# Performance work log

Hardware: AMD Instinct MI355X
Metric: run time of the kernel (lower is better)

## Reference

```python
import jax, jax.numpy as jnp
import numpy as np

N_HEADS = 8
N_POINTS = 4


def _bilinear_sample(img, x, y):
    """img: (d, H, W); x, y: (P, H, W) float pixel coords (align_corners=True).
    Zero padding for out-of-bounds (matches F.grid_sample defaults).
    Returns (d, P, H, W)."""
    Hh, Ww = img.shape[1], img.shape[2]
    x0f = jnp.floor(x); y0f = jnp.floor(y)
    x0 = x0f.astype(jnp.int32); x1 = x0 + 1
    y0 = y0f.astype(jnp.int32); y1 = y0 + 1
    wx = x - x0f; wy = y - y0f

    def gather(yi, xi):
        valid = (yi >= 0) & (yi < Hh) & (xi >= 0) & (xi < Ww)
        yc = jnp.clip(yi, 0, Hh - 1)
        xc = jnp.clip(xi, 0, Ww - 1)
        v = img[:, yc, xc]  # (d, P, H, W)
        return v * valid[None].astype(img.dtype)

    out = (gather(y0, x0) * ((1 - wy) * (1 - wx))[None]
           + gather(y0, x1) * ((1 - wy) * wx)[None]
           + gather(y1, x0) * (wy * (1 - wx))[None]
           + gather(y1, x1) * (wy * wx)[None])
    return out


def _forward(query, key, W_off, b_off, W_proj, b_proj):
    B, C, H, W = query.shape
    nh, npts = N_HEADS, N_POINTS
    dh = C // nh
    N = H * W

    # offsets + weights from flattened query tokens
    qf = query.reshape(B, C, N).transpose(0, 2, 1)            # (B, N, C)
    ow = qf @ W_off + b_off                                    # (B, N, nh*npts*3)
    ow = ow.reshape(B, H, W, nh, npts, 3)
    offsets = ow[..., :2]                                      # (B,H,W,nh,npts,2)
    weights = jax.nn.softmax(ow[..., 2], axis=-1)              # (B,H,W,nh,npts)

    # base grid in [-1, 1], (x, y) order
    gy = jnp.linspace(-1.0, 1.0, H, dtype=query.dtype)
    gx = jnp.linspace(-1.0, 1.0, W, dtype=query.dtype)
    gyy, gxx = jnp.meshgrid(gy, gx, indexing='ij')             # (H, W)
    grid = jnp.stack([gxx, gyy], axis=-1)                      # (H, W, 2)

    locs = grid[None, :, :, None, None, :] + offsets * 0.1     # (B,H,W,nh,npts,2)
    locs = locs.transpose(0, 3, 4, 1, 2, 5)                    # (B,nh,npts,H,W,2)
    locs = locs.reshape(B * nh, npts, H, W, 2)

    # normalized -> pixel coords (align_corners=True)
    xpix = (locs[..., 0] + 1.0) * 0.5 * (W - 1)                # (B*nh, npts, H, W)
    ypix = (locs[..., 1] + 1.0) * 0.5 * (H - 1)

    key_r = key.reshape(B * nh, dh, H, W)
    sampled = jax.vmap(_bilinear_sample)(key_r, xpix, ypix)    # (B*nh, dh, npts, H, W)
    sampled = sampled.reshape(B, nh, dh, npts, H, W).transpose(0, 1, 3, 2, 4, 5)  # (B,nh,npts,dh,H,W)

    w = weights.transpose(0, 3, 4, 1, 2)[:, :, :, None, :, :]  # (B,nh,npts,1,H,W)
    out_feat = (sampled * w).sum(axis=2)                       # (B,nh,dh,H,W)
    out_feat = out_feat.reshape(B, C, N).transpose(0, 2, 1)    # (B,N,C)
    return out_feat @ W_proj + b_proj                          # (B,N,C)


def setup_inputs() -> dict:
    key0 = jax.random.key(0)
    ks = jax.random.split(key0, 6)
    B, C, H, W = 8, 256, 64, 64
    query = jax.random.normal(ks[0], (B, C, H, W), dtype=jnp.float32)
    key = jax.random.normal(ks[1], (B, C, H, W), dtype=jnp.float32)
    # small random offset net so sampling deviates from base grid (orig inits to 0)
    W_off = jax.random.normal(ks[2], (C, N_HEADS * N_POINTS * 3), dtype=jnp.float32) * 0.01
    b_off = jax.random.normal(ks[3], (N_HEADS * N_POINTS * 3,), dtype=jnp.float32) * 0.01
    W_proj = jax.random.normal(ks[4], (C, C), dtype=jnp.float32) * (1.0 / np.sqrt(C))
    b_proj = jnp.zeros((C,), dtype=jnp.float32)
    return {"query": query, "key": key, "W_off": W_off, "b_off": b_off,
            "W_proj": W_proj, "b_proj": b_proj}


def reference(query, key, W_off, b_off, W_proj, b_proj):
    return _forward(query, key, W_off, b_off, W_proj, b_proj)
```

## Files before the change

kernel.cpp:

```cpp
#include <hip/hip_runtime.h>

#define NH   8
#define NPTS 4
#define BB   8
#define CCH  256
#define HH   64
#define WW   64
#define NPIX 4096
#define DH   32

__global__ __launch_bounds__(256)
void kA_gemm(const float* __restrict__ query, const float* __restrict__ W_off,
             const float* __restrict__ b_off, float4* __restrict__ coords)
{
    __shared__ float a_lds[32][68];
    __shared__ float w_lds[32][100];

    const int t  = threadIdx.x;
    const int m0 = blockIdx.x * 64;
    const int b  = m0 >> 12;
    const int n0 = m0 & (NPIX - 1);
    const float* qbase = query + (size_t)b * CCH * NPIX + n0;

    const int tm = t >> 3;
    const int tj = t & 7;

    float acc[2][12];
#pragma unroll
    for (int i = 0; i < 2; ++i)
#pragma unroll
        for (int j = 0; j < 12; ++j) acc[i][j] = 0.f;

    for (int kc = 0; kc < CCH; kc += 32) {
        float4 a[2];
#pragma unroll
        for (int ii = 0; ii < 2; ++ii) {
            const int idx = t + ii * 256;
            a[ii] = *(const float4*)(qbase + (size_t)(kc + (idx >> 4)) * NPIX
                                     + ((idx & 15) << 2));
        }
        float4 w[3];
#pragma unroll
        for (int ii = 0; ii < 3; ++ii) {
            const int idx = t + ii * 256;
            const int kk = idx / 24, q = idx - kk * 24;
            w[ii] = *(const float4*)(W_off + (size_t)(kc + kk) * 96 + (q << 2));
        }
        __syncthreads();
#pragma unroll
        for (int ii = 0; ii < 2; ++ii) {
            const int idx = t + ii * 256;
            *(float4*)&a_lds[idx >> 4][(idx & 15) << 2] = a[ii];
        }
#pragma unroll
        for (int ii = 0; ii < 3; ++ii) {
            const int idx = t + ii * 256;
            const int kk = idx / 24, q = idx - kk * 24;
            *(float4*)&w_lds[kk][q << 2] = w[ii];
        }
        __syncthreads();
#pragma unroll
        for (int k = 0; k < 32; ++k) {
            const float2 av = *(const float2*)&a_lds[k][tm << 1];
            const float4 w0 = *(const float4*)&w_lds[k][tj * 12];
            const float4 w1 = *(const float4*)&w_lds[k][tj * 12 + 4];
            const float4 w2 = *(const float4*)&w_lds[k][tj * 12 + 8];
            const float ar[2]  = {av.x, av.y};
            const float wr[12] = {w0.x, w0.y, w0.z, w0.w,
                                  w1.x, w1.y, w1.z, w1.w,
                                  w2.x, w2.y, w2.z, w2.w};
#pragma unroll
            for (int i = 0; i < 2; ++i)
#pragma unroll
                for (int j = 0; j < 12; ++j)
                    acc[i][j] = fmaf(ar[i], wr[j], acc[i][j]);
        }
    }

    float bo[12];
#pragma unroll
    for (int j = 0; j < 12; ++j) bo[j] = b_off[tj * 12 + j];

#pragma unroll
    for (int i = 0; i < 2; ++i) {
        const int g = m0 + (tm << 1) + i;
        const int n = g & (NPIX - 1);
        const float fx = (float)(n & 63), fy = (float)(n >> 6);

        float ox[4], oy[4], l[4];
#pragma unroll
        for (int p = 0; p < 4; ++p) {
            ox[p] = acc[i][p * 3 + 0] + bo[p * 3 + 0];
            oy[p] = acc[i][p * 3 + 1] + bo[p * 3 + 1];
            l[p]  = acc[i][p * 3 + 2] + bo[p * 3 + 2];
        }
        float m = fmaxf(fmaxf(l[0], l[1]), fmaxf(l[2], l[3]));
        float e[4], s = 0.f;
#pragma unroll
        for (int p = 0; p < 4; ++p) { e[p] = __expf(l[p] - m); s += e[p]; }
        const float inv = 1.f / s;

        float4* cp = coords + ((size_t)g * NH + tj) * NPTS;
#pragma unroll
        for (int p = 0; p < 4; ++p)
            cp[p] = make_float4(fx + ox[p] * 3.15f, fy + oy[p] * 3.15f,
                                e[p] * inv, 0.f);
    }
}

__global__ __launch_bounds__(256)
void kT_transpose(const float* __restrict__ key, float* __restrict__ keyT)
{
    __shared__ float tile[64][65];
    int bid = blockIdx.x;
    const int nt = bid & 63; bid >>= 6;
    const int ct = bid & 3;  bid >>= 2;
    const int b  = bid;
    const int n0 = nt * 64, c0 = ct * 64;
    const int t = threadIdx.x;

    const float* src = key + ((size_t)b * CCH + c0) * NPIX + n0;
#pragma unroll
    for (int ii = 0; ii < 4; ++ii) {
        int idx = t + ii * 256;
        int cc = idx >> 4, q = idx & 15;
        float4 v = *(const float4*)(src + (size_t)cc * NPIX + (q << 2));
        tile[cc][(q << 2) + 0] = v.x;
        tile[cc][(q << 2) + 1] = v.y;
        tile[cc][(q << 2) + 2] = v.z;
        tile[cc][(q << 2) + 3] = v.w;
    }
    __syncthreads();
    float* dst = keyT + ((size_t)(b * NPIX + n0)) * CCH + c0;
#pragma unroll
    for (int ii = 0; ii < 4; ++ii) {
        int idx = t + ii * 256;
        int nn = idx >> 4, q = idx & 15;
        float4 v = make_float4(tile[(q << 2) + 0][nn], tile[(q << 2) + 1][nn],
                               tile[(q << 2) + 2][nn], tile[(q << 2) + 3][nn]);
        *(float4*)(dst + (size_t)nn * CCH + (q << 2)) = v;
    }
}

__global__ __launch_bounds__(256)
void kB_gather(const float* __restrict__ keyT, const float4* __restrict__ coords,
               float* __restrict__ feat)
{
    const int bid  = blockIdx.x;
    const int sbid = (bid & 7) * 1024 + (bid >> 3);

    const int t  = threadIdx.x;
    const int wv = t >> 6, l = t & 63;
    const int g  = sbid * 4 + wv;
    const int b  = g >> 12;
    const int head = l >> 3;
    const int cl   = (l & 7) << 2;
    const int c    = head * DH + cl;

    const float*  kb = keyT + (((size_t)b << 12)) * CCH;
    const float4* cp = coords + ((size_t)g * NH + head) * NPTS;

    float4 acc = make_float4(0.f, 0.f, 0.f, 0.f);
#pragma unroll
    for (int pt = 0; pt < 4; ++pt) {
        float4 co = cp[pt];
        float xp = co.x, yp = co.y, wgt = co.z;
        float x0f = floorf(xp), y0f = floorf(yp);
        int   x0  = (int)x0f,  y0  = (int)y0f;
        float wx  = xp - x0f,  wy  = yp - y0f;
#pragma unroll
        for (int cr = 0; cr < 4; ++cr) {
            int   xi = x0 + (cr & 1);
            int   yi = y0 + (cr >> 1);
            float wc = ((cr & 1) ? wx : 1.f - wx) * ((cr >> 1) ? wy : 1.f - wy);
            bool  valid = (xi >= 0) && (xi < WW) && (yi >= 0) && (yi < HH);
            int   xc = min(max(xi, 0), WW - 1);
            int   yc = min(max(yi, 0), HH - 1);
            float ww = valid ? (wgt * wc) : 0.f;
            float4 v = *(const float4*)(kb + ((size_t)((yc << 6) + xc)) * CCH + c);
            acc.x = fmaf(ww, v.x, acc.x);
            acc.y = fmaf(ww, v.y, acc.y);
            acc.z = fmaf(ww, v.z, acc.z);
            acc.w = fmaf(ww, v.w, acc.w);
        }
    }
    *(float4*)(feat + (size_t)g * CCH + c) = acc;
}

__global__ __launch_bounds__(256)
void kB_sample(const float* __restrict__ key, const float4* __restrict__ coords,
               float* __restrict__ feat)
{
    __shared__ float cx[4][64], cy[4][64], cw[4][64];

    const int t = threadIdx.x;
    int bi = blockIdx.x;
    const int y    = bi & 63; bi >>= 6;
    const int head = bi & 7;  bi >>= 3;
    const int b    = bi;

    {
        const int xx = t >> 2, pt = t & 3;
        float4 v = coords[((size_t)(b * NPIX + y * WW + xx) * NH + head) * NPTS + pt];
        cx[pt][xx] = v.x; cy[pt][xx] = v.y; cw[pt][xx] = v.z;
    }
    __syncthreads();

    const int x  = t & 63;
    const int cg = t >> 6;
    const int c0 = head * DH + cg * 8;
    const float* kbase = key + ((size_t)b * CCH + c0) * NPIX;

    float acc[8];
#pragma unroll
    for (int i = 0; i < 8; ++i) acc[i] = 0.f;

#pragma unroll
    for (int pt = 0; pt < 4; ++pt) {
        float xp = cx[pt][x], yp = cy[pt][x], wgt = cw[pt][x];
        float x0f = floorf(xp), y0f = floorf(yp);
        int   x0  = (int)x0f,  y0  = (int)y0f;
        float wx  = xp - x0f,  wy  = yp - y0f;
#pragma unroll
        for (int cr = 0; cr < 4; ++cr) {
            int   xi = x0 + (cr & 1);
            int   yi = y0 + (cr >> 1);
            float wc = ((cr & 1) ? wx : 1.f - wx) * ((cr >> 1) ? wy : 1.f - wy);
            bool  valid = (xi >= 0) && (xi < WW) && (yi >= 0) && (yi < HH);
            int   xc = min(max(xi, 0), WW - 1);
            int   yc = min(max(yi, 0), HH - 1);
            const float* p = kbase + yc * WW + xc;
            float ww = valid ? (wgt * wc) : 0.f;
#pragma unroll
            for (int c = 0; c < 8; ++c)
                acc[c] = fmaf(ww, p[(size_t)c * NPIX], acc[c]);
        }
    }

    float* fp = feat + (size_t)(b * NPIX + y * WW + x) * CCH + c0;
    *(float4*)fp       = make_float4(acc[0], acc[1], acc[2], acc[3]);
    *(float4*)(fp + 4) = make_float4(acc[4], acc[5], acc[6], acc[7]);
}

__global__ __launch_bounds__(256)
void kC_proj(const float* __restrict__ feat, const float* __restrict__ W_proj,
             const float* __restrict__ b_proj, float* __restrict__ out)
{
    __shared__ float a_lds[32][68];
    __shared__ float b_lds[32][128];

    const int t  = threadIdx.x;
    const int mb = blockIdx.x >> 1;
    const int nb = blockIdx.x & 1;
    const int m0 = mb * 64, n0 = nb * 128;

    const int tm = t >> 4, tn = t & 15;
    const int ra = t >> 3, qa = t & 7;
    const int kb = t >> 5, qb = t & 31;

    float acc[4][8];
#pragma unroll
    for (int i = 0; i < 4; ++i)
#pragma unroll
        for (int j = 0; j < 8; ++j) acc[i][j] = 0.f;

    for (int kc = 0; kc < 256; kc += 32) {
        float4 a[2];
#pragma unroll
        for (int ii = 0; ii < 2; ++ii)
            a[ii] = *(const float4*)(feat + (size_t)(m0 + ra + ii * 32) * 256 + kc + (qa << 2));
        float4 w[4];
#pragma unroll
        for (int ii = 0; ii < 4; ++ii)
            w[ii] = *(const float4*)(W_proj + (size_t)(kc + kb + ii * 8) * 256 + n0 + (qb << 2));
        __syncthreads();
#pragma unroll
        for (int ii = 0; ii < 2; ++ii) {
            const int r = ra + ii * 32;
            a_lds[(qa << 2) + 0][r] = a[ii].x;
            a_lds[(qa << 2) + 1][r] = a[ii].y;
            a_lds[(qa << 2) + 2][r] = a[ii].z;
            a_lds[(qa << 2) + 3][r] = a[ii].w;
        }
#pragma unroll
        for (int ii = 0; ii < 4; ++ii)
            *(float4*)&b_lds[kb + ii * 8][qb << 2] = w[ii];
        __syncthreads();
#pragma unroll
        for (int k = 0; k < 32; ++k) {
            float4 av  = *(const float4*)&a_lds[k][tm << 2];
            float4 bv0 = *(const float4*)&b_lds[k][tn << 2];
            float4 bv1 = *(const float4*)&b_lds[k][64 + (tn << 2)];
            float ar[4] = {av.x, av.y, av.z, av.w};
            float br[8] = {bv0.x, bv0.y, bv0.z, bv0.w, bv1.x, bv1.y, bv1.z, bv1.w};
#pragma unroll
            for (int i = 0; i < 4; ++i)
#pragma unroll
                for (int j = 0; j < 8; ++j)
                    acc[i][j] = fmaf(ar[i], br[j], acc[i][j]);
        }
    }

    const float4 bp0 = *(const float4*)(b_proj + n0 + (tn << 2));
    const float4 bp1 = *(const float4*)(b_proj + n0 + 64 + (tn << 2));
#pragma unroll
    for (int i = 0; i < 4; ++i) {
        float* op = out + (size_t)(m0 + (tm << 2) + i) * 256 + n0;
        *(float4*)(op + (tn << 2)) =
            make_float4(acc[i][0] + bp0.x, acc[i][1] + bp0.y,
                        acc[i][2] + bp0.z, acc[i][3] + bp0.w);
        *(float4*)(op + 64 + (tn << 2)) =
            make_float4(acc[i][4] + bp1.x, acc[i][5] + bp1.y,
                        acc[i][6] + bp1.z, acc[i][7] + bp1.w);
    }
}

extern "C" void kernel_launch(void* const* d_in, const int* in_sizes, int n_in,
                              void* d_out, int out_size, void* d_ws, size_t ws_size,
                              hipStream_t stream)
{
    const float* query  = (const float*)d_in[0];
    const float* key    = (const float*)d_in[1];
    const float* W_off  = (const float*)d_in[2];
    const float* b_off  = (const float*)d_in[3];
    const float* W_proj = (const float*)d_in[4];
    const float* b_proj = (const float*)d_in[5];
    float* out = (float*)d_out;

    const size_t keyT_bytes   = (size_t)BB * NPIX * CCH * sizeof(float);
    const size_t coords_bytes = (size_t)BB * NPIX * NH * NPTS * sizeof(float4);
    const size_t feat_bytes   = (size_t)BB * NPIX * CCH * sizeof(float);

    if (ws_size >= keyT_bytes + coords_bytes + feat_bytes) {
        float*  keyT   = (float*)d_ws;
        float4* coords = (float4*)((char*)d_ws + keyT_bytes);
        float*  feat   = (float*)((char*)d_ws + keyT_bytes + coords_bytes);

        kA_gemm<<<(BB * NPIX) / 64, 256, 0, stream>>>(query, W_off, b_off, coords);
        kT_transpose<<<BB * 4 * 64, 256, 0, stream>>>(key, keyT);
        kB_gather<<<(BB * NPIX) / 4, 256, 0, stream>>>(keyT, coords, feat);
        kC_proj<<<(BB * NPIX / 64) * 2, 256, 0, stream>>>(feat, W_proj, b_proj, out);
    } else {
        float4* coords = (float4*)d_ws;
        float*  feat   = (float*)((char*)d_ws + coords_bytes);

        kA_gemm<<<(BB * NPIX) / 64, 256, 0, stream>>>(query, W_off, b_off, coords);
        kB_sample<<<BB * NH * HH, 256, 0, stream>>>(key, coords, feat);
        kC_proj<<<(BB * NPIX / 64) * 2, 256, 0, stream>>>(feat, W_proj, b_proj, out);
    }
}
```

Baseline: 257.1 us.

## Split-K offset GEMM across half-blocks and remap block order in both GEMMs

```diff
diff --git a/kernel.cpp b/kernel.cpp
--- a/kernel.cpp
+++ b/kernel.cpp
@@ -13,98 +13,132 @@
 void kA_gemm(const float* __restrict__ query, const float* __restrict__ W_off,
              const float* __restrict__ b_off, float4* __restrict__ coords)
 {
-    __shared__ float a_lds[32][68];
-    __shared__ float w_lds[32][100];
-
-    const int t  = threadIdx.x;
-    const int m0 = blockIdx.x * 64;
-    const int b  = m0 >> 12;
-    const int n0 = m0 & (NPIX - 1);
+    __shared__ float a_lds[64][68];
+    __shared__ float w_lds[64][100];
+
+    const int t    = threadIdx.x;
+    const int bid  = blockIdx.x;
+    const int sbid = (bid & 7) * 64 + (bid >> 3);
+    const int m0   = sbid * 64;
+    const int b    = m0 >> 12;
+    const int n0   = m0 & (NPIX - 1);
     const float* qbase = query + (size_t)b * CCH * NPIX + n0;
 
-    const int tm = t >> 3;
-    const int tj = t & 7;
-
-    float acc[2][12];
-#pragma unroll
-    for (int i = 0; i < 2; ++i)
+    const int kg = t >> 7;
+    const int tl = t & 127;
+    const int tm = tl >> 3;
+    const int tj = tl & 7;
+
+    float acc[4][12];
+#pragma unroll
+    for (int i = 0; i < 4; ++i)
 #pragma unroll
         for (int j = 0; j < 12; ++j) acc[i][j] = 0.f;
 
-    for (int kc = 0; kc < CCH; kc += 32) {
-        float4 a[2];
-#pragma unroll
-        for (int ii = 0; ii < 2; ++ii) {
-            const int idx = t + ii * 256;
-            a[ii] = *(const float4*)(qbase + (size_t)(kc + (idx >> 4)) * NPIX
-                                     + ((idx & 15) << 2));
-        }
-        float4 w[3];
-#pragma unroll
-        for (int ii = 0; ii < 3; ++ii) {
-            const int idx = t + ii * 256;
-            const int kk = idx / 24, q = idx - kk * 24;
-            w[ii] = *(const float4*)(W_off + (size_t)(kc + kk) * 96 + (q << 2));
+    for (int kc = 0; kc < 128; kc += 32) {
+        float4 a[4];
+#pragma unroll
+        for (int ii = 0; ii < 4; ++ii) {
+            const int idx = t + ii * 256;
+            const int lr = idx >> 4, m4 = idx & 15;
+            const int gk = ((lr >> 5) << 7) + kc + (lr & 31);
+            a[ii] = *(const float4*)(qbase + (size_t)gk * NPIX + (m4 << 2));
+        }
+        float4 w[6];
+#pragma unroll
+        for (int ii = 0; ii < 6; ++ii) {
+            const int idx = t + ii * 256;
+            const int lr = idx / 24, q = idx - lr * 24;
+            const int gk = ((lr >> 5) << 7) + kc + (lr & 31);
+            w[ii] = *(const float4*)(W_off + (size_t)gk * 96 + (q << 2));
         }
         __syncthreads();
 #pragma unroll
-        for (int ii = 0; ii < 2; ++ii) {
+        for (int ii = 0; ii < 4; ++ii) {
             const int idx = t + ii * 256;
             *(float4*)&a_lds[idx >> 4][(idx & 15) << 2] = a[ii];
         }
 #pragma unroll
-        for (int ii = 0; ii < 3; ++ii) {
-            const int idx = t + ii * 256;
-            const int kk = idx / 24, q = idx - kk * 24;
-            *(float4*)&w_lds[kk][q << 2] = w[ii];
+        for (int ii = 0; ii < 6; ++ii) {
+            const int idx = t + ii * 256;
+            const int lr = idx / 24, q = idx - lr * 24;
+            *(float4*)&w_lds[lr][q << 2] = w[ii];
         }
         __syncthreads();
-#pragma unroll
-        for (int k = 0; k < 32; ++k) {
-            const float2 av = *(const float2*)&a_lds[k][tm << 1];
-            const float4 w0 = *(const float4*)&w_lds[k][tj * 12];
-            const float4 w1 = *(const float4*)&w_lds[k][tj * 12 + 4];
-            const float4 w2 = *(const float4*)&w_lds[k][tj * 12 + 8];
-            const float ar[2]  = {av.x, av.y};
+
+        const int kr0 = kg << 5;
+#pragma unroll
+        for (int kk = 0; kk < 32; ++kk) {
+            const int kr = kr0 + kk;
+            const float4 av = *(const float4*)&a_lds[kr][tm << 2];
+            const float4 w0 = *(const float4*)&w_lds[kr][tj * 12];
+            const float4 w1 = *(const float4*)&w_lds[kr][tj * 12 + 4];
+            const float4 w2 = *(const float4*)&w_lds[kr][tj * 12 + 8];
+            const float ar[4]  = {av.x, av.y, av.z, av.w};
             const float wr[12] = {w0.x, w0.y, w0.z, w0.w,
                                   w1.x, w1.y, w1.z, w1.w,
                                   w2.x, w2.y, w2.z, w2.w};
 #pragma unroll
-            for (int i = 0; i < 2; ++i)
+            for (int i = 0; i < 4; ++i)
 #pragma unroll
                 for (int j = 0; j < 12; ++j)
                     acc[i][j] = fmaf(ar[i], wr[j], acc[i][j]);
         }
     }
 
-    float bo[12];
-#pragma unroll
-    for (int j = 0; j < 12; ++j) bo[j] = b_off[tj * 12 + j];
-
-#pragma unroll
-    for (int i = 0; i < 2; ++i) {
-        const int g = m0 + (tm << 1) + i;
-        const int n = g & (NPIX - 1);
-        const float fx = (float)(n & 63), fy = (float)(n >> 6);
-
-        float ox[4], oy[4], l[4];
-#pragma unroll
-        for (int p = 0; p < 4; ++p) {
-            ox[p] = acc[i][p * 3 + 0] + bo[p * 3 + 0];
-            oy[p] = acc[i][p * 3 + 1] + bo[p * 3 + 1];
-            l[p]  = acc[i][p * 3 + 2] + bo[p * 3 + 2];
-        }
-        float m = fmaxf(fmaxf(l[0], l[1]), fmaxf(l[2], l[3]));
-        float e[4], s = 0.f;
-#pragma unroll
-        for (int p = 0; p < 4; ++p) { e[p] = __expf(l[p] - m); s += e[p]; }
-        const float inv = 1.f / s;
-
-        float4* cp = coords + ((size_t)g * NH + tj) * NPTS;
-#pragma unroll
-        for (int p = 0; p < 4; ++p)
-            cp[p] = make_float4(fx + ox[p] * 3.15f, fy + oy[p] * 3.15f,
-                                e[p] * inv, 0.f);
+    __syncthreads();
+    if (kg == 0) {
+#pragma unroll
+        for (int i = 0; i < 4; ++i)
+#pragma unroll
+            for (int jq = 0; jq < 3; ++jq) {
+                float4 v = make_float4(acc[i][jq * 4 + 0], acc[i][jq * 4 + 1],
+                                       acc[i][jq * 4 + 2], acc[i][jq * 4 + 3]);
+                *(float4*)&w_lds[(tm << 2) + i][tj * 12 + (jq << 2)] = v;
+            }
+    }
+    __syncthreads();
+    if (kg == 1) {
+#pragma unroll
+        for (int i = 0; i < 4; ++i)
+#pragma unroll
+            for (int jq = 0; jq < 3; ++jq) {
+                const float4 v = *(const float4*)&w_lds[(tm << 2) + i][tj * 12 + (jq << 2)];
+                acc[i][jq * 4 + 0] += v.x;
+                acc[i][jq * 4 + 1] += v.y;
+                acc[i][jq * 4 + 2] += v.z;
+                acc[i][jq * 4 + 3] += v.w;
+            }
+
+        float bo[12];
+#pragma unroll
+        for (int j = 0; j < 12; ++j) bo[j] = b_off[tj * 12 + j];
+
+#pragma unroll
+        for (int i = 0; i < 4; ++i) {
+            const int g = m0 + (tm << 2) + i;
+            const int n = g & (NPIX - 1);
+            const float fx = (float)(n & 63), fy = (float)(n >> 6);
+
+            float ox[4], oy[4], l[4];
+#pragma unroll
+            for (int p = 0; p < 4; ++p) {
+                ox[p] = acc[i][p * 3 + 0] + bo[p * 3 + 0];
+                oy[p] = acc[i][p * 3 + 1] + bo[p * 3 + 1];
+                l[p]  = acc[i][p * 3 + 2] + bo[p * 3 + 2];
+            }
+            float m = fmaxf(fmaxf(l[0], l[1]), fmaxf(l[2], l[3]));
+            float e[4], s = 0.f;
+#pragma unroll
+            for (int p = 0; p < 4; ++p) { e[p] = __expf(l[p] - m); s += e[p]; }
+            const float inv = 1.f / s;
+
+            float4* cp = coords + ((size_t)g * NH + tj) * NPTS;
+#pragma unroll
+            for (int p = 0; p < 4; ++p)
+                cp[p] = make_float4(fx + ox[p] * 3.15f, fy + oy[p] * 3.15f,
+                                    e[p] * inv, 0.f);
+        }
     }
 }
 
@@ -246,17 +280,17 @@
 void kC_proj(const float* __restrict__ feat, const float* __restrict__ W_proj,
              const float* __restrict__ b_proj, float* __restrict__ out)
 {
-    __shared__ float a_lds[32][68];
+    __shared__ float a_lds[64][36];
     __shared__ float b_lds[32][128];
 
-    const int t  = threadIdx.x;
-    const int mb = blockIdx.x >> 1;
-    const int nb = blockIdx.x & 1;
+    const int t    = threadIdx.x;
+    const int bid  = blockIdx.x;
+    const int sbid = (bid & 7) * 128 + (bid >> 3);
+    const int mb = sbid >> 1;
+    const int nb = sbid & 1;
     const int m0 = mb * 64, n0 = nb * 128;
 
     const int tm = t >> 4, tn = t & 15;
-    const int ra = t >> 3, qa = t & 7;
-    const int kb = t >> 5, qb = t & 31;
 
     float acc[4][8];
 #pragma unroll
@@ -267,37 +301,51 @@
     for (int kc = 0; kc < 256; kc += 32) {
         float4 a[2];
 #pragma unroll
-        for (int ii = 0; ii < 2; ++ii)
-            a[ii] = *(const float4*)(feat + (size_t)(m0 + ra + ii * 32) * 256 + kc + (qa << 2));
+        for (int ii = 0; ii < 2; ++ii) {
+            const int idx = t + ii * 256;
+            a[ii] = *(const float4*)(feat + (size_t)(m0 + (idx >> 3)) * 256
+                                     + kc + ((idx & 7) << 2));
+        }
         float4 w[4];
 #pragma unroll
-        for (int ii = 0; ii < 4; ++ii)
-            w[ii] = *(const float4*)(W_proj + (size_t)(kc + kb + ii * 8) * 256 + n0 + (qb << 2));
+        for (int ii = 0; ii < 4; ++ii) {
+            const int idx = t + ii * 256;
+            w[ii] = *(const float4*)(W_proj + (size_t)(kc + (idx >> 5)) * 256
+                                     + n0 + ((idx & 31) << 2));
+        }
         __syncthreads();
 #pragma unroll
         for (int ii = 0; ii < 2; ++ii) {
-            const int r = ra + ii * 32;
-            a_lds[(qa << 2) + 0][r] = a[ii].x;
-            a_lds[(qa << 2) + 1][r] = a[ii].y;
-            a_lds[(qa << 2) + 2][r] = a[ii].z;
-            a_lds[(qa << 2) + 3][r] = a[ii].w;
-        }
-#pragma unroll
-        for (int ii = 0; ii < 4; ++ii)
-            *(float4*)&b_lds[kb + ii * 8][qb << 2] = w[ii];
+            const int idx = t + ii * 256;
+            *(float4*)&a_lds[idx >> 3][(idx & 7) << 2] = a[ii];
+        }
+#pragma unroll
+        for (int ii = 0; ii < 4; ++ii) {
+            const int idx = t + ii * 256;
+            *(float4*)&b_lds[idx >> 5][(idx & 31) << 2] = w[ii];
+        }
         __syncthreads();
 #pragma unroll
-        for (int k = 0; k < 32; ++k) {
-            float4 av  = *(const float4*)&a_lds[k][tm << 2];
-            float4 bv0 = *(const float4*)&b_lds[k][tn << 2];
-            float4 bv1 = *(const float4*)&b_lds[k][64 + (tn << 2)];
-            float ar[4] = {av.x, av.y, av.z, av.w};
-            float br[8] = {bv0.x, bv0.y, bv0.z, bv0.w, bv1.x, bv1.y, bv1.z, bv1.w};
-#pragma unroll
-            for (int i = 0; i < 4; ++i)
-#pragma unroll
-                for (int j = 0; j < 8; ++j)
-                    acc[i][j] = fmaf(ar[i], br[j], acc[i][j]);
+        for (int k4 = 0; k4 < 8; ++k4) {
+            float ar[4][4];
+#pragma unroll
+            for (int i = 0; i < 4; ++i) {
+                const float4 av = *(const float4*)&a_lds[(tm << 2) + i][k4 << 2];
+                ar[i][0] = av.x; ar[i][1] = av.y; ar[i][2] = av.z; ar[i][3] = av.w;
+            }
+#pragma unroll
+            for (int kk = 0; kk < 4; ++kk) {
+                const int k = (k4 << 2) + kk;
+                const float4 bv0 = *(const float4*)&b_lds[k][tn << 2];
+                const float4 bv1 = *(const float4*)&b_lds[k][64 + (tn << 2)];
+                const float br[8] = {bv0.x, bv0.y, bv0.z, bv0.w,
+                                     bv1.x, bv1.y, bv1.z, bv1.w};
+#pragma unroll
+                for (int i = 0; i < 4; ++i)
+#pragma unroll
+                    for (int j = 0; j < 8; ++j)
+                        acc[i][j] = fmaf(ar[i][kk], br[j], acc[i][j]);
+            }
         }
     }
 
```

Measured after the change: 269.9 us. 1.05x slower.
